# Optimization experiments

Hardware: AMD Instinct MI355X
Metric: run time of the kernel (lower is better)

## Reference

```python
import jax, jax.numpy as jnp
import numpy as np

H_GRID = 24
W_GRID = 24
NUM_HEADS = 3
FEAT_DIM = 192
HEAD_DIM = FEAT_DIM // NUM_HEADS  # 64
SCALE = HEAD_DIM ** -0.5
LN_EPS = 1e-5


def _positional():
    # matches get_positional_encodings with intrinsics=None; depends only on grid
    ys = jnp.linspace(-1.0, 1.0, H_GRID)
    xs = jnp.linspace(-1.0, 1.0, W_GRID)
    p3 = jnp.tile(ys, W_GRID)            # [N]
    p4 = jnp.repeat(xs, H_GRID)          # [N]
    p2 = p3 * p4
    p1 = p4 * p4
    p0 = p3 * p3
    return jnp.stack([p0, p1, p2, p3, p4, jnp.ones_like(p0)], axis=1)  # [N, 6]


def _layernorm(x, w, b):
    mu = jnp.mean(x, axis=-1, keepdims=True)
    var = jnp.mean((x - mu) ** 2, axis=-1, keepdims=True)
    return (x - mu) / jnp.sqrt(var + LN_EPS) * w + b


def _qkv_heads(x, qkv_w):
    # x: [B, N, C] -> q,k,v each [B, H, N, hd]
    B, N, _ = x.shape
    qkv = x @ qkv_w.T                                    # [B, N, 3*F]
    qkv = qkv.reshape(B, N, 3, NUM_HEADS, HEAD_DIM)
    qkv = jnp.transpose(qkv, (2, 0, 3, 1, 4))            # [3, B, H, N, hd]
    return qkv[0], qkv[1], qkv[2]


def _dual_softmax(attn):
    return jax.nn.softmax(attn, axis=-1) * jax.nn.softmax(attn, axis=-2)


def setup_inputs() -> dict:
    key = jax.random.key(0)
    ks = jax.random.split(key, 4)
    B, C = 64, 256
    in_dim, out_dim = C, 512
    dim_size = 2 * NUM_HEADS * (HEAD_DIM + 6) * (HEAD_DIM + 6)  # 29400
    return {
        "x1": jax.random.normal(ks[0], (B, C, H_GRID, W_GRID), jnp.float32),
        "x2": jax.random.normal(ks[1], (B, C, H_GRID, W_GRID), jnp.float32),
        "ln_w": jnp.ones((in_dim,), jnp.float32),
        "ln_b": jnp.zeros((in_dim,), jnp.float32),
        "qkv_w": jax.random.normal(ks[2], (3 * FEAT_DIM, in_dim), jnp.float32) * (in_dim ** -0.5),
        "proj_w": jax.random.normal(ks[3], (out_dim, dim_size), jnp.float32) * (dim_size ** -0.5),
        "proj_b": jnp.zeros((out_dim,), jnp.float32),
    }


def reference(x1, x2, ln_w, ln_b, qkv_w, proj_w, proj_b):
    B, C, h, w = x1.shape
    N = h * w
    x1t = _layernorm(x1.reshape(B, C, N).transpose(0, 2, 1), ln_w, ln_b)  # [B, N, C]
    x2t = _layernorm(x2.reshape(B, C, N).transpose(0, 2, 1), ln_w, ln_b)

    q1, k1, v1 = _qkv_heads(x1t, qkv_w)
    q2, k2, v2 = _qkv_heads(x2t, qkv_w)

    attn_1 = jnp.einsum("bhnd,bhmd->bhnm", q2, k1) * SCALE
    attn_2 = jnp.einsum("bhnd,bhmd->bhnm", q1, k2) * SCALE
    af1 = _dual_softmax(attn_1)
    af2 = _dual_softmax(attn_2)

    pos = jnp.broadcast_to(_positional(), (B, NUM_HEADS, N, 6))
    v1p = jnp.concatenate([v1, pos], axis=-1)  # [B, H, N, hd+6]
    v2p = jnp.concatenate([v2, pos], axis=-1)

    f1 = jnp.einsum("bhnd,bhnm,bhme->bhde", v1p, af1, v1p)  # [B, H, hd+6, hd+6]
    f2 = jnp.einsum("bhnd,bhnm,bhme->bhde", v2p, af2, v2p)

    feat = jnp.concatenate([f1.reshape(B, -1), f2.reshape(B, -1)], axis=-1)
    return jax.nn.relu(feat @ proj_w.T + proj_b)
```

## Files before the change

kernel.cpp:

```cpp
#include <hip/hip_runtime.h>

#define NSEQ 576
#define CDIM 256
#define HEADS 3
#define HD 64
#define FEAT 192
#define QKVF 576
#define QK_F 384
#define VP 70
#define BHN 192
#define DIMSZ 29400

typedef __attribute__((ext_vector_type(8))) _Float16 half8;
typedef __attribute__((ext_vector_type(4))) _Float16 half4;
typedef __attribute__((ext_vector_type(4))) float f32x4;

#define MFMA16(A,B,C) __builtin_amdgcn_mfma_f32_16x16x32_f16(A,B,C,0,0,0)

__device__ __forceinline__ float posval(int n, int pe){
  int yi = n % 24, xi = n / 24;
  float py = (float)yi * (2.0f/23.0f) - 1.0f;
  float px = (float)xi * (2.0f/23.0f) - 1.0f;
  switch(pe){
    case 0: return py*py;
    case 1: return px*px;
    case 2: return py*px;
    case 3: return py;
    case 4: return px;
    default: return 1.0f;
  }
}

template<int LD>
__device__ __forceinline__ half8 fragT(const _Float16 (*s)[LD], int row, int dbase){
  half4 a = *(const half4*)&s[row][dbase];
  half4 b = *(const half4*)&s[row][dbase + 16];
  return __builtin_shufflevector(a, b, 0, 1, 2, 3, 4, 5, 6, 7);
}

__device__ __forceinline__ void stage_copy64(const _Float16* __restrict__ src, int rstr,
                                             _Float16 (*d)[72], int t){
  #pragma unroll
  for (int k2 = 0; k2 < 2; ++k2){
    int idx = t + 256 * k2;
    int row = idx >> 3, c = (idx & 7) << 3;
    half8 v = *(const half8*)(src + (size_t)row * rstr + c);
    *(half4*)&d[row][c]     = (half4){v[0], v[1], v[2], v[3]};
    *(half4*)&d[row][c + 4] = (half4){v[4], v[5], v[6], v[7]};
  }
}

__global__ __launch_bounds__(192) void k_ln_stats(const float* __restrict__ x1, const float* __restrict__ x2,
                                                  float* __restrict__ mu, float* __restrict__ rstd){
  int idx = blockIdx.x;
  int i2 = idx / 192;
  int rem = idx % 192;
  int b = rem / 3, ng = rem % 3;
  int n = ng * 192 + threadIdx.x;
  const float* x = i2 ? x2 : x1;
  const float* xb = x + (size_t)b * CDIM * NSEQ + n;
  float s = 0.f, sq = 0.f;
  for (int c = 0; c < CDIM; ++c){
    float v = xb[(size_t)c * NSEQ];
    s += v; sq += v * v;
  }
  float m = s * (1.0f/256.0f);
  float var = sq * (1.0f/256.0f) - m * m;
  int o = (i2 * 64 + b) * NSEQ + n;
  mu[o] = m;
  rstd[o] = rsqrtf(var + 1e-5f);
}

__global__ __launch_bounds__(256) void k_qkv_gemm_mfma(const float* __restrict__ x1, const float* __restrict__ x2,
                                                       const float* __restrict__ mu, const float* __restrict__ rstd,
                                                       const float* __restrict__ lnw, const float* __restrict__ lnb,
                                                       const float* __restrict__ qkvw,
                                                       _Float16* __restrict__ qh, _Float16* __restrict__ ql,
                                                       _Float16* __restrict__ vpTh, _Float16* __restrict__ vpTl){
  int wg = (blockIdx.x & 7) * 1296 + (blockIdx.x >> 3);
  int ft = wg % 9;
  int mt = wg / 9;
  int ibn = mt * 64;
  int i2 = ibn / (64 * NSEQ);
  int bn = ibn % (64 * NSEQ);
  int b  = bn / NSEQ;
  int n0 = bn % NSEQ;
  const float* x = i2 ? x2 : x1;
  const float* xb = x + (size_t)b * CDIM * NSEQ + n0;
  __shared__ __align__(16) _Float16 Xh[64][68];
  __shared__ __align__(16) _Float16 Xl[64][68];
  __shared__ __align__(16) _Float16 Wh[64][68];
  __shared__ __align__(16) _Float16 Wl[64][68];
  __shared__ float smu[64], srstd[64], slnw[256], slnb[256];
  int t = threadIdx.x;
  int w = t >> 6, lane = t & 63, tx = lane & 15, hi = lane >> 4;
  if (t < 64){ smu[t] = mu[ibn + t]; srstd[t] = rstd[ibn + t]; }
  slnw[t] = lnw[t]; slnb[t] = lnb[t];

  f32x4 acc[4];
  #pragma unroll
  for (int s = 0; s < 4; ++s) acc[s] = (f32x4){0.f, 0.f, 0.f, 0.f};

  int nA = t & 63, cg = t >> 6;
  int fr = t >> 2, cq = t & 3;
  for (int c0 = 0; c0 < CDIM; c0 += 64){
    __syncthreads();
    float mun = smu[nA], rsn = srstd[nA];
    #pragma unroll
    for (int rr = 0; rr < 16; ++rr){
      int c = cg * 16 + rr;
      float v = xb[(size_t)(c0 + c) * NSEQ + nA];
      float xv = (v - mun) * rsn * slnw[c0 + c] + slnb[c0 + c];
      _Float16 hh = (_Float16)xv;
      Xh[nA][c] = hh;
      Xl[nA][c] = (_Float16)(xv - (float)hh);
    }
    const float* wp = qkvw + (size_t)(ft * 64 + fr) * CDIM + c0 + cq * 16;
    #pragma unroll
    for (int rr = 0; rr < 4; ++rr){
      float4 wv = *(const float4*)(wp + rr * 4);
      half4 h, l;
      h.x = (_Float16)wv.x; l.x = (_Float16)(wv.x - (float)h.x);
      h.y = (_Float16)wv.y; l.y = (_Float16)(wv.y - (float)h.y);
      h.z = (_Float16)wv.z; l.z = (_Float16)(wv.z - (float)h.z);
      h.w = (_Float16)wv.w; l.w = (_Float16)(wv.w - (float)h.w);
      *(half4*)&Wh[fr][cq * 16 + rr * 4] = h;
      *(half4*)&Wl[fr][cq * 16 + rr * 4] = l;
    }
    __syncthreads();
    #pragma unroll
    for (int kc = 0; kc < 2; ++kc){
      half8 wh = fragT<68>(Wh, w * 16 + tx, kc * 32 + hi * 4);
      half8 wl = fragT<68>(Wl, w * 16 + tx, kc * 32 + hi * 4);
      #pragma unroll
      for (int s = 0; s < 4; ++s){
        half8 xh = fragT<68>(Xh, s * 16 + tx, kc * 32 + hi * 4);
        half8 xl = fragT<68>(Xl, s * 16 + tx, kc * 32 + hi * 4);
        acc[s] = MFMA16(xh, wh, acc[s]);
        acc[s] = MFMA16(xl, wh, acc[s]);
        acc[s] = MFMA16(xh, wl, acc[s]);
      }
    }
  }
  if (ft < 6){
    #pragma unroll
    for (int s = 0; s < 4; ++s)
      #pragma unroll
      for (int rr = 0; rr < 4; ++rr){
        float v = acc[s][rr];
        _Float16 hh = (_Float16)v;
        size_t o = (size_t)(ibn + s * 16 + hi * 4 + rr) * QK_F + ft * 64 + w * 16 + tx;
        qh[o] = hh;
        ql[o] = (_Float16)(v - (float)hh);
      }
  } else {
    __syncthreads();
    #pragma unroll
    for (int s = 0; s < 4; ++s)
      #pragma unroll
      for (int rr = 0; rr < 4; ++rr){
        float v = acc[s][rr];
        _Float16 hh = (_Float16)v;
        Xh[s * 16 + hi * 4 + rr][w * 16 + tx] = hh;
        Xl[s * 16 + hi * 4 + rr][w * 16 + tx] = (_Float16)(v - (float)hh);
      }
    __syncthreads();
    int mbg = i2 * 192 + b * 3 + (ft - 6);
    #pragma unroll
    for (int it = 0; it < 16; ++it){
      int d = (t >> 6) + it * 4;
      int n2 = t & 63;
      size_t o = ((size_t)mbg * 80 + d) * NSEQ + n0 + n2;
      vpTh[o] = Xh[n2][d];
      vpTl[o] = Xl[n2][d];
    }
  }
}

__global__ __launch_bounds__(256) void k_pos_fill(_Float16* __restrict__ vpTh, _Float16* __restrict__ vpTl){
  int idx = blockIdx.x * 256 + threadIdx.x;
  if (idx >= 384 * 16 * NSEQ) return;
  int n = idx % NSEQ;
  int r = idx / NSEQ;
  int row = 64 + (r & 15);
  int mb = r >> 4;
  float v = 0.f;
  int pe = row - 64;
  if (pe < 6) v = posval(n, pe);
  _Float16 hh = (_Float16)v;
  size_t o = ((size_t)mb * 80 + row) * NSEQ + n;
  vpTh[o] = hh;
  vpTl[o] = (_Float16)(v - (float)hh);
}

__global__ __launch_bounds__(256) void k_attn_stats_mfma(const _Float16* __restrict__ qh, const _Float16* __restrict__ ql,
                                                         float* __restrict__ rs, float* __restrict__ cs_part){
  int wg = (blockIdx.x & 7) * 432 + (blockIdx.x >> 3);
  int map = wg / (BHN * 9);
  int r   = wg % (BHN * 9);
  int bh = r / 9, nt = r % 9;
  int b = bh / 3, h = bh % 3;
  int qi = 1 - map, ki = map;
  int mb = map * BHN + bh;
  const _Float16* qbh = qh + (size_t)((qi * 64 + b) * NSEQ) * QK_F + h * HD;
  const _Float16* qbl = ql + (size_t)((qi * 64 + b) * NSEQ) * QK_F + h * HD;
  const _Float16* kbh = qh + (size_t)((ki * 64 + b) * NSEQ) * QK_F + FEAT + h * HD;
  const _Float16* kbl = ql + (size_t)((ki * 64 + b) * NSEQ) * QK_F + FEAT + h * HD;
  int n0 = nt * 64;
  __shared__ __align__(16) _Float16 Ash[64][72];
  __shared__ __align__(16) _Float16 Asl[64][72];
  __shared__ float cpart[4][64];
  int t = threadIdx.x;
  int w = t >> 6, lane = t & 63, tx = lane & 15, hi = lane >> 4;

  stage_copy64(qbh + (size_t)n0 * QK_F, QK_F, Ash, t);
  stage_copy64(qbl + (size_t)n0 * QK_F, QK_F, Asl, t);
  __syncthreads();
  half8 qh0 = fragT<72>(Ash, w * 16 + tx, 0 + hi * 4);
  half8 qh1 = fragT<72>(Ash, w * 16 + tx, 32 + hi * 4);
  half8 ql0 = fragT<72>(Asl, w * 16 + tx, 0 + hi * 4);
  half8 ql1 = fragT<72>(Asl, w * 16 + tx, 32 + hi * 4);

  float rsum = 0.f;
  for (int mt = 0; mt < 9; ++mt){
    int m0 = mt * 64;
    __syncthreads();
    stage_copy64(kbh + (size_t)m0 * QK_F, QK_F, Ash, t);
    stage_copy64(kbl + (size_t)m0 * QK_F, QK_F, Asl, t);
    __syncthreads();
    f32x4 acc[4];
    #pragma unroll
    for (int s = 0; s < 4; ++s) acc[s] = (f32x4){0.f, 0.f, 0.f, 0.f};
    #pragma unroll
    for (int s = 0; s < 4; ++s){
      half8 kh0 = fragT<72>(Ash, s * 16 + tx, 0 + hi * 4);
      half8 kl0 = fragT<72>(Asl, s * 16 + tx, 0 + hi * 4);
      half8 kh1 = fragT<72>(Ash, s * 16 + tx, 32 + hi * 4);
      half8 kl1 = fragT<72>(Asl, s * 16 + tx, 32 + hi * 4);
      acc[s] = MFMA16(kh0, qh0, acc[s]);
      acc[s] = MFMA16(kl0, qh0, acc[s]);
      acc[s] = MFMA16(kh0, ql0, acc[s]);
      acc[s] = MFMA16(kh1, qh1, acc[s]);
      acc[s] = MFMA16(kl1, qh1, acc[s]);
      acc[s] = MFMA16(kh1, ql1, acc[s]);
    }
    #pragma unroll
    for (int s = 0; s < 4; ++s){
      #pragma unroll
      for (int rr = 0; rr < 4; ++rr){
        float e = __expf(acc[s][rr] * 0.125f);
        rsum += e;
        float c = e;
        c += __shfl_xor(c, 1);
        c += __shfl_xor(c, 2);
        c += __shfl_xor(c, 4);
        c += __shfl_xor(c, 8);
        if (tx == 0) cpart[w][s * 16 + hi * 4 + rr] = c;
      }
    }
    __syncthreads();
    if (t < 64){
      float s2 = cpart[0][t] + cpart[1][t] + cpart[2][t] + cpart[3][t];
      cs_part[((size_t)mb * 9 + nt) * NSEQ + m0 + t] = s2;
    }
  }
  rsum += __shfl_xor(rsum, 16);
  rsum += __shfl_xor(rsum, 32);
  if (lane < 16) rs[(size_t)mb * NSEQ + n0 + w * 16 + lane] = rsum;
}

__global__ __launch_bounds__(256) void k_cs_reduce(const float* __restrict__ cs_part, float* __restrict__ cs){
  int tid = blockIdx.x * 256 + threadIdx.x;
  if (tid >= 2 * BHN * NSEQ) return;
  int mb = tid / NSEQ, m = tid % NSEQ;
  float s = 0.f;
  #pragma unroll
  for (int p = 0; p < 9; ++p)
    s += cs_part[((size_t)mb * 9 + p) * NSEQ + m];
  cs[tid] = s;
}

__global__ __launch_bounds__(256) void k_apply_mfma(const _Float16* __restrict__ qh, const _Float16* __restrict__ ql,
                                                    const _Float16* __restrict__ vpTh, const _Float16* __restrict__ vpTl,
                                                    const float* __restrict__ rs, const float* __restrict__ cs,
                                                    _Float16* __restrict__ tTh, _Float16* __restrict__ tTl, int map){
  int wg = (blockIdx.x & 7) * 216 + (blockIdx.x >> 3);
  int bh = wg / 9, nt = wg % 9;
  int b = bh / 3, h = bh % 3;
  int qi = 1 - map, ki = map;
  int mb = map * BHN + bh;
  const _Float16* qbh = qh + (size_t)((qi * 64 + b) * NSEQ) * QK_F + h * HD;
  const _Float16* qbl = ql + (size_t)((qi * 64 + b) * NSEQ) * QK_F + h * HD;
  const _Float16* kbh = qh + (size_t)((ki * 64 + b) * NSEQ) * QK_F + FEAT + h * HD;
  const _Float16* kbl = ql + (size_t)((ki * 64 + b) * NSEQ) * QK_F + FEAT + h * HD;
  const _Float16* vTh = vpTh + (size_t)mb * 80 * NSEQ;
  const _Float16* vTl = vpTl + (size_t)mb * 80 * NSEQ;
  int n0 = nt * 64;
  __shared__ __align__(16) _Float16 Ash[64][72];
  __shared__ __align__(16) _Float16 Asl[64][72];
  __shared__ __align__(16) _Float16 Vth[80][72];
  __shared__ __align__(16) _Float16 Vtl[80][72];
  __shared__ float cinv[64];
  int t = threadIdx.x;
  int w = t >> 6, lane = t & 63, tx = lane & 15, hi = lane >> 4;

  stage_copy64(qbh + (size_t)n0 * QK_F, QK_F, Ash, t);
  stage_copy64(qbl + (size_t)n0 * QK_F, QK_F, Asl, t);
  __syncthreads();
  half8 qh0 = fragT<72>(Ash, w * 16 + tx, 0 + hi * 4);
  half8 qh1 = fragT<72>(Ash, w * 16 + tx, 32 + hi * 4);
  half8 ql0 = fragT<72>(Asl, w * 16 + tx, 0 + hi * 4);
  half8 ql1 = fragT<72>(Asl, w * 16 + tx, 32 + hi * 4);
  float rinv = 1.0f / rs[(size_t)mb * NSEQ + n0 + w * 16 + tx];

  f32x4 tacc[5];
  #pragma unroll
  for (int et = 0; et < 5; ++et) tacc[et] = (f32x4){0.f, 0.f, 0.f, 0.f};

  for (int mt = 0; mt < 9; ++mt){
    int m0 = mt * 64;
    __syncthreads();
    stage_copy64(kbh + (size_t)m0 * QK_F, QK_F, Ash, t);
    stage_copy64(kbl + (size_t)m0 * QK_F, QK_F, Asl, t);
    #pragma unroll
    for (int k2 = 0; k2 < 3; ++k2){
      int idx = t + 256 * k2;
      if (idx < 640){
        int row = idx >> 3, c = (idx & 7) << 3;
        half8 v1 = *(const half8*)(vTh + (size_t)row * NSEQ + m0 + c);
        *(half4*)&Vth[row][c]     = (half4){v1[0], v1[1], v1[2], v1[3]};
        *(half4*)&Vth[row][c + 4] = (half4){v1[4], v1[5], v1[6], v1[7]};
        half8 v2 = *(const half8*)(vTl + (size_t)row * NSEQ + m0 + c);
        *(half4*)&Vtl[row][c]     = (half4){v2[0], v2[1], v2[2], v2[3]};
        *(half4*)&Vtl[row][c + 4] = (half4){v2[4], v2[5], v2[6], v2[7]};
      }
    }
    if (t < 64) cinv[t] = 1.0f / cs[(size_t)mb * NSEQ + m0 + t];
    __syncthreads();

    f32x4 acc[4];
    #pragma unroll
    for (int s = 0; s < 4; ++s) acc[s] = (f32x4){0.f, 0.f, 0.f, 0.f};
    #pragma unroll
    for (int s = 0; s < 4; ++s){
      half8 kh0 = fragT<72>(Ash, s * 16 + tx, 0 + hi * 4);
      half8 kl0 = fragT<72>(Asl, s * 16 + tx, 0 + hi * 4);
      half8 kh1 = fragT<72>(Ash, s * 16 + tx, 32 + hi * 4);
      half8 kl1 = fragT<72>(Asl, s * 16 + tx, 32 + hi * 4);
      acc[s] = MFMA16(kh0, qh0, acc[s]);
      acc[s] = MFMA16(kl0, qh0, acc[s]);
      acc[s] = MFMA16(kh0, ql0, acc[s]);
      acc[s] = MFMA16(kh1, qh1, acc[s]);
      acc[s] = MFMA16(kl1, qh1, acc[s]);
      acc[s] = MFMA16(kh1, ql1, acc[s]);
    }
    half8 bhf[2], blf[2];
    #pragma unroll
    for (int s = 0; s < 4; ++s){
      #pragma unroll
      for (int rr = 0; rr < 4; ++rr){
        float e2 = __expf(acc[s][rr] * 0.25f);
        float af = e2 * rinv * cinv[s * 16 + hi * 4 + rr];
        _Float16 hh = (_Float16)af;
        _Float16 ll = (_Float16)(af - (float)hh);
        bhf[s >> 1][(s & 1) * 4 + rr] = hh;
        blf[s >> 1][(s & 1) * 4 + rr] = ll;
      }
    }
    #pragma unroll
    for (int et = 0; et < 5; ++et){
      #pragma unroll
      for (int mc = 0; mc < 2; ++mc){
        half8 vhf = fragT<72>(Vth, et * 16 + tx, mc * 32 + hi * 4);
        half8 vlf = fragT<72>(Vtl, et * 16 + tx, mc * 32 + hi * 4);
        tacc[et] = MFMA16(vhf, bhf[mc], tacc[et]);
        tacc[et] = MFMA16(vhf, blf[mc], tacc[et]);
        tacc[et] = MFMA16(vlf, bhf[mc], tacc[et]);
      }
    }
  }
  #pragma unroll
  for (int et = 0; et < 5; ++et){
    #pragma unroll
    for (int rr = 0; rr < 4; ++rr){
      int e = et * 16 + hi * 4 + rr;
      float v = tacc[et][rr];
      _Float16 hh = (_Float16)v;
      size_t o = ((size_t)bh * 80 + e) * NSEQ + n0 + w * 16 + tx;
      tTh[o] = hh;
      tTl[o] = (_Float16)(v - (float)hh);
    }
  }
}

__global__ __launch_bounds__(256) void k_f_gemm_mfma(const _Float16* __restrict__ vpTh, const _Float16* __restrict__ vpTl,
                                                     const _Float16* __restrict__ tTh, const _Float16* __restrict__ tTl,
                                                     float* __restrict__ featT3, int map){
  int wg = blockIdx.x;
  int mbL = wg / 3, part = wg % 3;
  int b = mbL / 3, h = mbL % 3;
  __shared__ __align__(16) _Float16 Ah[80][40], Al[80][40], Bh[80][40], Bl[80][40];
  int t = threadIdx.x;
  int w4 = t >> 6, lane = t & 63, tx = lane & 15, hi = lane >> 4;
  const _Float16* Abh = vpTh + (size_t)(map * BHN + mbL) * 80 * NSEQ;
  const _Float16* Abl = vpTl + (size_t)(map * BHN + mbL) * 80 * NSEQ;
  const _Float16* Bbh = tTh + (size_t)mbL * 80 * NSEQ;
  const _Float16* Bbl = tTl + (size_t)mbL * 80 * NSEQ;
  f32x4 acc[7];
  #pragma unroll
  for (int j = 0; j < 7; ++j) acc[j] = (f32x4){0.f, 0.f, 0.f, 0.f};

  for (int kc = part * 6; kc < part * 6 + 6; ++kc){
    int c0 = kc * 32;
    __syncthreads();
    #pragma unroll
    for (int k2 = 0; k2 < 2; ++k2){
      int idx = t + 256 * k2;
      if (idx < 320){
        int row = idx >> 2, cc = (idx & 3) << 3;
        *(half8*)&Ah[row][cc] = *(const half8*)(Abh + (size_t)row * NSEQ + c0 + cc);
        *(half8*)&Al[row][cc] = *(const half8*)(Abl + (size_t)row * NSEQ + c0 + cc);
        *(half8*)&Bh[row][cc] = *(const half8*)(Bbh + (size_t)row * NSEQ + c0 + cc);
        *(half8*)&Bl[row][cc] = *(const half8*)(Bbl + (size_t)row * NSEQ + c0 + cc);
      }
    }
    __syncthreads();
    #pragma unroll
    for (int j = 0; j < 7; ++j){
      int ti = w4 + 4 * j;
      if (ti < 25){
        int db = ti / 5, eb = ti % 5;
        half8 ah = *(const half8*)&Ah[db * 16 + tx][hi * 8];
        half8 al = *(const half8*)&Al[db * 16 + tx][hi * 8];
        half8 bh = *(const half8*)&Bh[eb * 16 + tx][hi * 8];
        half8 bl = *(const half8*)&Bl[eb * 16 + tx][hi * 8];
        acc[j] = MFMA16(ah, bh, acc[j]);
        acc[j] = MFMA16(al, bh, acc[j]);
        acc[j] = MFMA16(ah, bl, acc[j]);
      }
    }
  }
  #pragma unroll
  for (int j = 0; j < 7; ++j){
    int ti = w4 + 4 * j;
    if (ti < 25){
      int db = ti / 5, eb = ti % 5;
      #pragma unroll
      for (int rr = 0; rr < 4; ++rr){
        int d = db * 16 + hi * 4 + rr, e = eb * 16 + tx;
        if (d < VP && e < VP)
          featT3[(size_t)part * 1881600 + (size_t)(map * 14700 + h * 4900 + d * VP + e) * 64 + b] = acc[j][rr];
      }
    }
  }
}

__global__ __launch_bounds__(256) void k_feat_reduce(const float* __restrict__ featT3, float* __restrict__ featT){
  int gid = blockIdx.x * 256 + threadIdx.x;
  if (gid >= DIMSZ * 64) return;
  featT[gid] = featT3[gid] + featT3[1881600 + gid] + featT3[2 * 1881600 + gid];
}

__global__ __launch_bounds__(256) void k_proj_gemm(const float* __restrict__ featT, const float* __restrict__ pw,
                                                   float* __restrict__ p){
  int ot = blockIdx.x & 7;
  int s  = blockIdx.x >> 3;
  int o0 = ot * 64;
  int kbase = s * 300;
  __shared__ __align__(16) float As[20][72];
  __shared__ __align__(16) float Bs[20][72];
  int t = threadIdx.x, tx = t & 15, ty = t >> 4;
  float acc[4][4] = {};
  for (int kt = 0; kt < 15; ++kt){
    int k0 = kbase + kt * 20;
    __syncthreads();
    #pragma unroll
    for (int r = 0; r < 5; ++r){
      int idx = t + 256 * r;
      int bb = idx & 63, kk = idx >> 6;
      As[kk][bb] = featT[(size_t)(k0 + kk) * 64 + bb];
      int ko = idx % 20, oo = idx / 20;
      Bs[ko][oo] = pw[(size_t)(o0 + oo) * DIMSZ + k0 + ko];
    }
    __syncthreads();
    #pragma unroll
    for (int k = 0; k < 20; ++k){
      float4 a4 = *(const float4*)&As[k][ty * 4];
      float4 b4 = *(const float4*)&Bs[k][tx * 4];
      float aa[4] = {a4.x, a4.y, a4.z, a4.w};
      float bb[4] = {b4.x, b4.y, b4.z, b4.w};
      #pragma unroll
      for (int i = 0; i < 4; ++i)
        #pragma unroll
        for (int j = 0; j < 4; ++j)
          acc[i][j] += aa[i] * bb[j];
    }
  }
  int slice = s * 8 + ot;
  #pragma unroll
  for (int i = 0; i < 4; ++i){
    float4 st = make_float4(acc[i][0], acc[i][1], acc[i][2], acc[i][3]);
    *(float4*)&p[(size_t)slice * 4096 + (ty * 4 + i) * 64 + tx * 4] = st;
  }
}

__global__ __launch_bounds__(256) void k_finalize(const float* __restrict__ p, const float* __restrict__ pb,
                                                  float* __restrict__ out){
  int gid = blockIdx.x * 256 + threadIdx.x;
  int o = gid & 511, b = gid >> 9;
  int ot = o >> 6, lo = o & 63;
  float s = pb[o];
  for (int s2 = 0; s2 < 98; ++s2)
    s += p[(size_t)(s2 * 8 + ot) * 4096 + b * 64 + lo];
  out[gid] = fmaxf(s, 0.0f);
}

extern "C" void kernel_launch(void* const* d_in, const int* in_sizes, int n_in,
                              void* d_out, int out_size, void* d_ws, size_t ws_size,
                              hipStream_t stream) {
  const float* x1   = (const float*)d_in[0];
  const float* x2   = (const float*)d_in[1];
  const float* lnw  = (const float*)d_in[2];
  const float* lnb  = (const float*)d_in[3];
  const float* qkvw = (const float*)d_in[4];
  const float* pw   = (const float*)d_in[5];
  const float* pb   = (const float*)d_in[6];
  float* out = (float*)d_out;

  float* w = (float*)d_ws;
  float*     mu      = w;
  float*     rstd    = w + 73728;
  _Float16*  qh      = (_Float16*)(w + 147456);
  _Float16*  ql      = (_Float16*)(w + 14303232);
  _Float16*  vpTh    = (_Float16*)(w + 28459008);
  _Float16*  vpTl    = (_Float16*)(w + 37306368);
  _Float16*  tTh     = (_Float16*)(w + 46153728);
  _Float16*  tTl     = (_Float16*)(w + 50577408);
  float*     cs_part = w + 55001088;
  float*     featT   = w + 55001088;
  float*     rs      = w + 56991744;
  float*     cs      = w + 57212928;
  float*     featT3  = w + 57434112;
  float*     p       = w + 57434112;

  k_ln_stats<<<384, 192, 0, stream>>>(x1, x2, mu, rstd);
  k_qkv_gemm_mfma<<<10368, 256, 0, stream>>>(x1, x2, mu, rstd, lnw, lnb, qkvw, qh, ql, vpTh, vpTl);
  k_pos_fill<<<13824, 256, 0, stream>>>(vpTh, vpTl);
  k_attn_stats_mfma<<<3456, 256, 0, stream>>>(qh, ql, rs, cs_part);
  k_cs_reduce<<<864, 256, 0, stream>>>(cs_part, cs);
  for (int map = 0; map < 2; ++map){
    k_apply_mfma<<<1728, 256, 0, stream>>>(qh, ql, vpTh, vpTl, rs, cs, tTh, tTl, map);
    k_f_gemm_mfma<<<576, 256, 0, stream>>>(vpTh, vpTl, tTh, tTl, featT3, map);
  }
  k_feat_reduce<<<7350, 256, 0, stream>>>(featT3, featT);
  k_proj_gemm<<<784, 256, 0, stream>>>(featT, pw, p);
  k_finalize<<<128, 256, 0, stream>>>(p, pb, out);
}
```

Measured before the change: 763.6 us.

## Swizzle LDS tiles, enlarge apply query tile, restructure stats MFMA loop

Replaces padded LDS staging with a rotated (XOR-like) 64-column layout written as full half8 stores. In the stats kernel, the Q fragments for all four 16-row slices are held in registers, each wave owns one key slice, and the column-sum reduction moves from a cross-lane shuffle plus LDS to a cheap per-wave reduction. The apply kernel now uses 384 threads covering 192 query rows per block, with each wave computing two 16-row tiles. This amortises K/V tile loads over three times as many queries, at the cost of more registers and fewer blocks.

```diff
diff --git a/kernel.cpp b/kernel.cpp
--- a/kernel.cpp
+++ b/kernel.cpp
@@ -38,16 +38,8 @@
   return __builtin_shufflevector(a, b, 0, 1, 2, 3, 4, 5, 6, 7);
 }
 
-__device__ __forceinline__ void stage_copy64(const _Float16* __restrict__ src, int rstr,
-                                             _Float16 (*d)[72], int t){
-  #pragma unroll
-  for (int k2 = 0; k2 < 2; ++k2){
-    int idx = t + 256 * k2;
-    int row = idx >> 3, c = (idx & 7) << 3;
-    half8 v = *(const half8*)(src + (size_t)row * rstr + c);
-    *(half4*)&d[row][c]     = (half4){v[0], v[1], v[2], v[3]};
-    *(half4*)&d[row][c + 4] = (half4){v[4], v[5], v[6], v[7]};
-  }
+__device__ __forceinline__ int rotIdx(int row, int c16){
+  return row * 64 + ((((c16) + row) & 7) << 3);
 }
 
 __global__ __launch_bounds__(192) void k_ln_stats(const float* __restrict__ x1, const float* __restrict__ x2,
@@ -207,66 +199,81 @@
   const _Float16* kbh = qh + (size_t)((ki * 64 + b) * NSEQ) * QK_F + FEAT + h * HD;
   const _Float16* kbl = ql + (size_t)((ki * 64 + b) * NSEQ) * QK_F + FEAT + h * HD;
   int n0 = nt * 64;
-  __shared__ __align__(16) _Float16 Ash[64][72];
-  __shared__ __align__(16) _Float16 Asl[64][72];
-  __shared__ float cpart[4][64];
+  __shared__ __align__(16) _Float16 Kh[64 * 64];
+  __shared__ __align__(16) _Float16 Kl[64 * 64];
+  __shared__ float rsLds[4][64];
   int t = threadIdx.x;
   int w = t >> 6, lane = t & 63, tx = lane & 15, hi = lane >> 4;
 
-  stage_copy64(qbh + (size_t)n0 * QK_F, QK_F, Ash, t);
-  stage_copy64(qbl + (size_t)n0 * QK_F, QK_F, Asl, t);
+  for (int idx = t; idx < 1024; idx += 256){
+    int a = idx >> 9, rc = idx & 511, row = rc >> 3, c16 = rc & 7;
+    const _Float16* src = a ? qbl : qbh;
+    _Float16* dst = a ? Kl : Kh;
+    *(half8*)(dst + rotIdx(row, c16)) = *(const half8*)(src + (size_t)(n0 + row) * QK_F + c16 * 8);
+  }
   __syncthreads();
-  half8 qh0 = fragT<72>(Ash, w * 16 + tx, 0 + hi * 4);
-  half8 qh1 = fragT<72>(Ash, w * 16 + tx, 32 + hi * 4);
-  half8 ql0 = fragT<72>(Asl, w * 16 + tx, 0 + hi * 4);
-  half8 ql1 = fragT<72>(Asl, w * 16 + tx, 32 + hi * 4);
-
-  float rsum = 0.f;
+  half8 qAh[4][2], qAl[4][2];
+  #pragma unroll
+  for (int s = 0; s < 4; ++s)
+    #pragma unroll
+    for (int kc = 0; kc < 2; ++kc){
+      qAh[s][kc] = *(half8*)(Kh + rotIdx(s * 16 + tx, kc * 4 + hi));
+      qAl[s][kc] = *(half8*)(Kl + rotIdx(s * 16 + tx, kc * 4 + hi));
+    }
+
+  float rsum[4][4] = {};
   for (int mt = 0; mt < 9; ++mt){
     int m0 = mt * 64;
     __syncthreads();
-    stage_copy64(kbh + (size_t)m0 * QK_F, QK_F, Ash, t);
-    stage_copy64(kbl + (size_t)m0 * QK_F, QK_F, Asl, t);
+    for (int idx = t; idx < 1024; idx += 256){
+      int a = idx >> 9, rc = idx & 511, row = rc >> 3, c16 = rc & 7;
+      const _Float16* src = a ? kbl : kbh;
+      _Float16* dst = a ? Kl : Kh;
+      *(half8*)(dst + rotIdx(row, c16)) = *(const half8*)(src + (size_t)(m0 + row) * QK_F + c16 * 8);
+    }
     __syncthreads();
     f32x4 acc[4];
     #pragma unroll
     for (int s = 0; s < 4; ++s) acc[s] = (f32x4){0.f, 0.f, 0.f, 0.f};
     #pragma unroll
-    for (int s = 0; s < 4; ++s){
-      half8 kh0 = fragT<72>(Ash, s * 16 + tx, 0 + hi * 4);
-      half8 kl0 = fragT<72>(Asl, s * 16 + tx, 0 + hi * 4);
-      half8 kh1 = fragT<72>(Ash, s * 16 + tx, 32 + hi * 4);
-      half8 kl1 = fragT<72>(Asl, s * 16 + tx, 32 + hi * 4);
-      acc[s] = MFMA16(kh0, qh0, acc[s]);
-      acc[s] = MFMA16(kl0, qh0, acc[s]);
-      acc[s] = MFMA16(kh0, ql0, acc[s]);
-      acc[s] = MFMA16(kh1, qh1, acc[s]);
-      acc[s] = MFMA16(kl1, qh1, acc[s]);
-      acc[s] = MFMA16(kh1, ql1, acc[s]);
-    }
-    #pragma unroll
-    for (int s = 0; s < 4; ++s){
+    for (int kc = 0; kc < 2; ++kc){
+      half8 kb8 = *(half8*)(Kh + rotIdx(w * 16 + tx, kc * 4 + hi));
+      half8 kl8 = *(half8*)(Kl + rotIdx(w * 16 + tx, kc * 4 + hi));
+      #pragma unroll
+      for (int s = 0; s < 4; ++s){
+        acc[s] = MFMA16(qAh[s][kc], kb8, acc[s]);
+        acc[s] = MFMA16(qAl[s][kc], kb8, acc[s]);
+        acc[s] = MFMA16(qAh[s][kc], kl8, acc[s]);
+      }
+    }
+    float csum = 0.f;
+    #pragma unroll
+    for (int s = 0; s < 4; ++s)
       #pragma unroll
       for (int rr = 0; rr < 4; ++rr){
         float e = __expf(acc[s][rr] * 0.125f);
-        rsum += e;
-        float c = e;
-        c += __shfl_xor(c, 1);
-        c += __shfl_xor(c, 2);
-        c += __shfl_xor(c, 4);
-        c += __shfl_xor(c, 8);
-        if (tx == 0) cpart[w][s * 16 + hi * 4 + rr] = c;
-      }
-    }
-    __syncthreads();
-    if (t < 64){
-      float s2 = cpart[0][t] + cpart[1][t] + cpart[2][t] + cpart[3][t];
-      cs_part[((size_t)mb * 9 + nt) * NSEQ + m0 + t] = s2;
-    }
-  }
-  rsum += __shfl_xor(rsum, 16);
-  rsum += __shfl_xor(rsum, 32);
-  if (lane < 16) rs[(size_t)mb * NSEQ + n0 + w * 16 + lane] = rsum;
+        rsum[s][rr] += e;
+        csum += e;
+      }
+    csum += __shfl_xor(csum, 16);
+    csum += __shfl_xor(csum, 32);
+    if (lane < 16)
+      cs_part[((size_t)mb * 9 + nt) * NSEQ + m0 + w * 16 + tx] = csum;
+  }
+  #pragma unroll
+  for (int s = 0; s < 4; ++s)
+    #pragma unroll
+    for (int rr = 0; rr < 4; ++rr){
+      float v = rsum[s][rr];
+      v += __shfl_xor(v, 1);
+      v += __shfl_xor(v, 2);
+      v += __shfl_xor(v, 4);
+      v += __shfl_xor(v, 8);
+      if (tx == 0) rsLds[w][s * 16 + hi * 4 + rr] = v;
+    }
+  __syncthreads();
+  if (t < 64)
+    rs[(size_t)mb * NSEQ + n0 + t] = rsLds[0][t] + rsLds[1][t] + rsLds[2][t] + rsLds[3][t];
 }
 
 __global__ __launch_bounds__(256) void k_cs_reduce(const float* __restrict__ cs_part, float* __restrict__ cs){
@@ -280,12 +287,12 @@
   cs[tid] = s;
 }
 
-__global__ __launch_bounds__(256) void k_apply_mfma(const _Float16* __restrict__ qh, const _Float16* __restrict__ ql,
-                                                    const _Float16* __restrict__ vpTh, const _Float16* __restrict__ vpTl,
-                                                    const float* __restrict__ rs, const float* __restrict__ cs,
-                                                    _Float16* __restrict__ tTh, _Float16* __restrict__ tTl, int map){
-  int wg = (blockIdx.x & 7) * 216 + (blockIdx.x >> 3);
-  int bh = wg / 9, nt = wg % 9;
+__global__ __launch_bounds__(384, 2) void k_apply_mfma(const _Float16* __restrict__ qh, const _Float16* __restrict__ ql,
+                                                       const _Float16* __restrict__ vpTh, const _Float16* __restrict__ vpTl,
+                                                       const float* __restrict__ rs, const float* __restrict__ cs,
+                                                       _Float16* __restrict__ tTh, _Float16* __restrict__ tTl, int map){
+  int wg = (blockIdx.x & 7) * 72 + (blockIdx.x >> 3);
+  int bh = wg / 3, nt = wg % 3;
   int b = bh / 3, h = bh % 3;
   int qi = 1 - map, ki = map;
   int mb = map * BHN + bh;
@@ -295,102 +302,129 @@
   const _Float16* kbl = ql + (size_t)((ki * 64 + b) * NSEQ) * QK_F + FEAT + h * HD;
   const _Float16* vTh = vpTh + (size_t)mb * 80 * NSEQ;
   const _Float16* vTl = vpTl + (size_t)mb * 80 * NSEQ;
-  int n0 = nt * 64;
-  __shared__ __align__(16) _Float16 Ash[64][72];
-  __shared__ __align__(16) _Float16 Asl[64][72];
+  int n0 = nt * 192;
+  __shared__ __align__(16) _Float16 QLh[192 * 64];
+  __shared__ __align__(16) _Float16 QLl[192 * 64];
   __shared__ __align__(16) _Float16 Vth[80][72];
   __shared__ __align__(16) _Float16 Vtl[80][72];
   __shared__ float cinv[64];
   int t = threadIdx.x;
   int w = t >> 6, lane = t & 63, tx = lane & 15, hi = lane >> 4;
 
-  stage_copy64(qbh + (size_t)n0 * QK_F, QK_F, Ash, t);
-  stage_copy64(qbl + (size_t)n0 * QK_F, QK_F, Asl, t);
+  for (int idx = t; idx < 3072; idx += 384){
+    int a = idx / 1536, rc = idx % 1536;
+    int row = rc >> 3, c16 = rc & 7;
+    const _Float16* src = a ? qbl : qbh;
+    _Float16* dst = a ? QLl : QLh;
+    *(half8*)(dst + rotIdx(row, c16)) = *(const half8*)(src + (size_t)(n0 + row) * QK_F + c16 * 8);
+  }
   __syncthreads();
-  half8 qh0 = fragT<72>(Ash, w * 16 + tx, 0 + hi * 4);
-  half8 qh1 = fragT<72>(Ash, w * 16 + tx, 32 + hi * 4);
-  half8 ql0 = fragT<72>(Asl, w * 16 + tx, 0 + hi * 4);
-  half8 ql1 = fragT<72>(Asl, w * 16 + tx, 32 + hi * 4);
-  float rinv = 1.0f / rs[(size_t)mb * NSEQ + n0 + w * 16 + tx];
-
-  f32x4 tacc[5];
-  #pragma unroll
-  for (int et = 0; et < 5; ++et) tacc[et] = (f32x4){0.f, 0.f, 0.f, 0.f};
+  half8 qB0h[2], qB0l[2], qB1h[2], qB1l[2];
+  #pragma unroll
+  for (int kc = 0; kc < 2; ++kc){
+    qB0h[kc] = *(half8*)(QLh + rotIdx((2 * w + 0) * 16 + tx, kc * 4 + hi));
+    qB0l[kc] = *(half8*)(QLl + rotIdx((2 * w + 0) * 16 + tx, kc * 4 + hi));
+    qB1h[kc] = *(half8*)(QLh + rotIdx((2 * w + 1) * 16 + tx, kc * 4 + hi));
+    qB1l[kc] = *(half8*)(QLl + rotIdx((2 * w + 1) * 16 + tx, kc * 4 + hi));
+  }
+  float rinv0 = 1.0f / rs[(size_t)mb * NSEQ + n0 + (2 * w + 0) * 16 + tx];
+  float rinv1 = 1.0f / rs[(size_t)mb * NSEQ + n0 + (2 * w + 1) * 16 + tx];
+
+  f32x4 tacc0[5], tacc1[5];
+  #pragma unroll
+  for (int et = 0; et < 5; ++et){
+    tacc0[et] = (f32x4){0.f, 0.f, 0.f, 0.f};
+    tacc1[et] = (f32x4){0.f, 0.f, 0.f, 0.f};
+  }
 
   for (int mt = 0; mt < 9; ++mt){
     int m0 = mt * 64;
     __syncthreads();
-    stage_copy64(kbh + (size_t)m0 * QK_F, QK_F, Ash, t);
-    stage_copy64(kbl + (size_t)m0 * QK_F, QK_F, Asl, t);
-    #pragma unroll
-    for (int k2 = 0; k2 < 3; ++k2){
-      int idx = t + 256 * k2;
-      if (idx < 640){
-        int row = idx >> 3, c = (idx & 7) << 3;
-        half8 v1 = *(const half8*)(vTh + (size_t)row * NSEQ + m0 + c);
-        *(half4*)&Vth[row][c]     = (half4){v1[0], v1[1], v1[2], v1[3]};
-        *(half4*)&Vth[row][c + 4] = (half4){v1[4], v1[5], v1[6], v1[7]};
-        half8 v2 = *(const half8*)(vTl + (size_t)row * NSEQ + m0 + c);
-        *(half4*)&Vtl[row][c]     = (half4){v2[0], v2[1], v2[2], v2[3]};
-        *(half4*)&Vtl[row][c + 4] = (half4){v2[4], v2[5], v2[6], v2[7]};
-      }
+    for (int idx = t; idx < 1024; idx += 384){
+      int a = idx >> 9, rc = idx & 511, row = rc >> 3, c16 = rc & 7;
+      const _Float16* src = a ? kbl : kbh;
+      _Float16* dst = a ? QLl : QLh;
+      *(half8*)(dst + rotIdx(row, c16)) = *(const half8*)(src + (size_t)(m0 + row) * QK_F + c16 * 8);
+    }
+    for (int idx = t; idx < 1280; idx += 384){
+      int a = idx >= 640 ? 1 : 0;
+      int rc = idx - a * 640;
+      int row = rc >> 3, c16 = rc & 7;
+      const _Float16* src = a ? vTl : vTh;
+      _Float16* dst = a ? &Vtl[0][0] : &Vth[0][0];
+      *(half8*)(dst + row * 72 + c16 * 8) = *(const half8*)(src + (size_t)row * NSEQ + m0 + c16 * 8);
     }
     if (t < 64) cinv[t] = 1.0f / cs[(size_t)mb * NSEQ + m0 + t];
     __syncthreads();
 
-    f32x4 acc[4];
-    #pragma unroll
-    for (int s = 0; s < 4; ++s) acc[s] = (f32x4){0.f, 0.f, 0.f, 0.f};
+    f32x4 a0[4], a1[4];
     #pragma unroll
     for (int s = 0; s < 4; ++s){
-      half8 kh0 = fragT<72>(Ash, s * 16 + tx, 0 + hi * 4);
-      half8 kl0 = fragT<72>(Asl, s * 16 + tx, 0 + hi * 4);
-      half8 kh1 = fragT<72>(Ash, s * 16 + tx, 32 + hi * 4);
-      half8 kl1 = fragT<72>(Asl, s * 16 + tx, 32 + hi * 4);
-      acc[s] = MFMA16(kh0, qh0, acc[s]);
-      acc[s] = MFMA16(kl0, qh0, acc[s]);
-      acc[s] = MFMA16(kh0, ql0, acc[s]);
-      acc[s] = MFMA16(kh1, qh1, acc[s]);
-      acc[s] = MFMA16(kl1, qh1, acc[s]);
-      acc[s] = MFMA16(kh1, ql1, acc[s]);
-    }
-    half8 bhf[2], blf[2];
-    #pragma unroll
-    for (int s = 0; s < 4; ++s){
+      a0[s] = (f32x4){0.f, 0.f, 0.f, 0.f};
+      a1[s] = (f32x4){0.f, 0.f, 0.f, 0.f};
+    }
+    #pragma unroll
+    for (int kc = 0; kc < 2; ++kc)
+      #pragma unroll
+      for (int s = 0; s < 4; ++s){
+        half8 kh8 = *(half8*)(QLh + rotIdx(s * 16 + tx, kc * 4 + hi));
+        half8 kl8 = *(half8*)(QLl + rotIdx(s * 16 + tx, kc * 4 + hi));
+        a0[s] = MFMA16(kh8, qB0h[kc], a0[s]);
+        a0[s] = MFMA16(kl8, qB0h[kc], a0[s]);
+        a0[s] = MFMA16(kh8, qB0l[kc], a0[s]);
+        a1[s] = MFMA16(kh8, qB1h[kc], a1[s]);
+        a1[s] = MFMA16(kl8, qB1h[kc], a1[s]);
+        a1[s] = MFMA16(kh8, qB1l[kc], a1[s]);
+      }
+    half8 b0h[2], b0l[2], b1h[2], b1l[2];
+    #pragma unroll
+    for (int s = 0; s < 4; ++s)
       #pragma unroll
       for (int rr = 0; rr < 4; ++rr){
-        float e2 = __expf(acc[s][rr] * 0.25f);
-        float af = e2 * rinv * cinv[s * 16 + hi * 4 + rr];
-        _Float16 hh = (_Float16)af;
-        _Float16 ll = (_Float16)(af - (float)hh);
-        bhf[s >> 1][(s & 1) * 4 + rr] = hh;
-        blf[s >> 1][(s & 1) * 4 + rr] = ll;
-      }
-    }
-    #pragma unroll
-    for (int et = 0; et < 5; ++et){
+        float ci = cinv[s * 16 + hi * 4 + rr];
+        float af0 = __expf(a0[s][rr] * 0.25f) * rinv0 * ci;
+        _Float16 h0 = (_Float16)af0;
+        b0h[s >> 1][(s & 1) * 4 + rr] = h0;
+        b0l[s >> 1][(s & 1) * 4 + rr] = (_Float16)(af0 - (float)h0);
+        float af1 = __expf(a1[s][rr] * 0.25f) * rinv1 * ci;
+        _Float16 h1 = (_Float16)af1;
+        b1h[s >> 1][(s & 1) * 4 + rr] = h1;
+        b1l[s >> 1][(s & 1) * 4 + rr] = (_Float16)(af1 - (float)h1);
+      }
+    #pragma unroll
+    for (int et = 0; et < 5; ++et)
       #pragma unroll
       for (int mc = 0; mc < 2; ++mc){
         half8 vhf = fragT<72>(Vth, et * 16 + tx, mc * 32 + hi * 4);
         half8 vlf = fragT<72>(Vtl, et * 16 + tx, mc * 32 + hi * 4);
-        tacc[et] = MFMA16(vhf, bhf[mc], tacc[et]);
-        tacc[et] = MFMA16(vhf, blf[mc], tacc[et]);
-        tacc[et] = MFMA16(vlf, bhf[mc], tacc[et]);
-      }
-    }
-  }
-  #pragma unroll
-  for (int et = 0; et < 5; ++et){
+        tacc0[et] = MFMA16(vhf, b0h[mc], tacc0[et]);
+        tacc0[et] = MFMA16(vhf, b0l[mc], tacc0[et]);
+        tacc0[et] = MFMA16(vlf, b0h[mc], tacc0[et]);
+        tacc1[et] = MFMA16(vhf, b1h[mc], tacc1[et]);
+        tacc1[et] = MFMA16(vhf, b1l[mc], tacc1[et]);
+        tacc1[et] = MFMA16(vlf, b1h[mc], tacc1[et]);
+      }
+  }
+  #pragma unroll
+  for (int et = 0; et < 5; ++et)
     #pragma unroll
     for (int rr = 0; rr < 4; ++rr){
       int e = et * 16 + hi * 4 + rr;
-      float v = tacc[et][rr];
-      _Float16 hh = (_Float16)v;
-      size_t o = ((size_t)bh * 80 + e) * NSEQ + n0 + w * 16 + tx;
-      tTh[o] = hh;
-      tTl[o] = (_Float16)(v - (float)hh);
-    }
-  }
+      {
+        float v = tacc0[et][rr];
+        _Float16 hh = (_Float16)v;
+        size_t o = ((size_t)bh * 80 + e) * NSEQ + n0 + (2 * w + 0) * 16 + tx;
+        tTh[o] = hh;
+        tTl[o] = (_Float16)(v - (float)hh);
+      }
+      {
+        float v = tacc1[et][rr];
+        _Float16 hh = (_Float16)v;
+        size_t o = ((size_t)bh * 80 + e) * NSEQ + n0 + (2 * w + 1) * 16 + tx;
+        tTh[o] = hh;
+        tTl[o] = (_Float16)(v - (float)hh);
+      }
+    }
 }
 
 __global__ __launch_bounds__(256) void k_f_gemm_mfma(const _Float16* __restrict__ vpTh, const _Float16* __restrict__ vpTl,
@@ -549,7 +583,7 @@
   k_attn_stats_mfma<<<3456, 256, 0, stream>>>(qh, ql, rs, cs_part);
   k_cs_reduce<<<864, 256, 0, stream>>>(cs_part, cs);
   for (int map = 0; map < 2; ++map){
-    k_apply_mfma<<<1728, 256, 0, stream>>>(qh, ql, vpTh, vpTl, rs, cs, tTh, tTl, map);
+    k_apply_mfma<<<576, 384, 0, stream>>>(qh, ql, vpTh, vpTl, rs, cs, tTh, tTl, map);
     k_f_gemm_mfma<<<576, 256, 0, stream>>>(vpTh, vpTl, tTh, tTl, featT3, map);
   }
   k_feat_reduce<<<7350, 256, 0, stream>>>(featT3, featT);
```

Result: slower. 836.1 us (+9.5%).
